# Kernel optimization log

Hardware: AMD Instinct MI355X
Metric: run time of the kernel (lower is better)

The kernel has to match this reference:

```python
import jax, jax.numpy as jnp
import numpy as np

EMBED_DIM = 4096
N_HEADS = 32
N_KV_HEADS = N_HEADS // 2
HEAD_DIM = EMBED_DIM // N_HEADS
MAX_SEQ_LEN = 4096


def setup_inputs() -> dict:
    key = jax.random.key(0)
    k1, k2, k3, k4, k5 = jax.random.split(key, 5)
    b, s = 1, 2048
    x = jax.random.normal(k1, (b, s, EMBED_DIM), dtype=jnp.float32)
    # rotary frequencies: theta=10000, angles[t, i] = t * 10000^{-2i/head_dim}
    inv_freq = 1.0 / (10000.0 ** (np.arange(0, HEAD_DIM, 2, dtype=np.float32) / HEAD_DIM))
    t = np.arange(MAX_SEQ_LEN, dtype=np.float32)
    ang = np.outer(t, inv_freq)  # [max_seq, head_dim/2]
    freqs_cis = jnp.asarray(np.stack([np.cos(ang), np.sin(ang)], axis=-1))  # [max_seq, hd/2, 2]
    scale = 0.02
    wq = jax.random.normal(k2, (EMBED_DIM, EMBED_DIM), dtype=jnp.float32) * scale
    wk = jax.random.normal(k3, (EMBED_DIM, N_KV_HEADS * HEAD_DIM), dtype=jnp.float32) * scale
    wv = jax.random.normal(k4, (EMBED_DIM, N_KV_HEADS * HEAD_DIM), dtype=jnp.float32) * scale
    wo = jax.random.normal(k5, (EMBED_DIM, EMBED_DIM), dtype=jnp.float32) * scale
    return {"x": x, "freqs_cis": freqs_cis, "wq": wq, "wk": wk, "wv": wv, "wo": wo, "start_pos": 0}


def _apply_rope(t, cos, sin):
    # t: [b, s, h, hd]; cos/sin: [1, s, 1, hd/2]
    tr = t.reshape(*t.shape[:-1], HEAD_DIM // 2, 2)
    t0, t1 = tr[..., 0], tr[..., 1]
    o0 = t0 * cos - t1 * sin
    o1 = t0 * sin + t1 * cos
    return jnp.stack([o0, o1], axis=-1).reshape(t.shape)


def reference(x, freqs_cis, wq, wk, wv, wo, start_pos):
    b, s, _ = x.shape
    q = (x @ wq).reshape(b, s, N_HEADS, HEAD_DIM)
    k = (x @ wk).reshape(b, s, N_KV_HEADS, HEAD_DIM)
    v = (x @ wv).reshape(b, s, N_KV_HEADS, HEAD_DIM)
    rep = N_HEADS // N_KV_HEADS
    k = jnp.repeat(k, rep, axis=2)  # GQA: expand KV heads (matches repeat_interleave)
    v = jnp.repeat(v, rep, axis=2)
    fc = freqs_cis[start_pos:start_pos + s]  # [s, hd/2, 2]
    cos = fc[None, :, None, :, 0]
    sin = fc[None, :, None, :, 1]
    q = _apply_rope(q, cos, sin)
    k = _apply_rope(k, cos, sin)
    # [b, h, s, hd]
    q = q.transpose(0, 2, 1, 3)
    k = k.transpose(0, 2, 1, 3)
    v = v.transpose(0, 2, 1, 3)
    scale = 1.0 / jnp.sqrt(jnp.float32(HEAD_DIM))
    scores = jnp.einsum("bhqd,bhkd->bhqk", q, k) * scale
    causal = jnp.tril(jnp.ones((s, s), dtype=bool))
    scores = jnp.where(causal[None, None], scores, jnp.finfo(scores.dtype).min)
    probs = jax.nn.softmax(scores, axis=-1)
    out = jnp.einsum("bhqk,bhkd->bhqd", probs, v)
    out = out.transpose(0, 2, 1, 3).reshape(b, s, EMBED_DIM)
    return out @ wo
```

## Files before the change

kernel.cpp:

```cpp
#include <hip/hip_runtime.h>
#include <stdint.h>

typedef unsigned short u16;
typedef __bf16 bf16x8 __attribute__((ext_vector_type(8)));
typedef float f32x4 __attribute__((ext_vector_type(4)));

#define SEQ   2048
#define EMBED 4096
#define KDIM  4096
#define NH    32
#define NKV   16
#define HD    128
#define KVW   2048

__device__ __forceinline__ float bf2f(u16 u) {
  union { uint32_t u; float f; } v; v.u = ((uint32_t)u) << 16; return v.f;
}
__device__ __forceinline__ u16 f2bf(float f) {
  union { float f; uint32_t u; } v; v.f = f;
  return (u16)((v.u + 0x7FFFu + ((v.u >> 16) & 1u)) >> 16);
}
__device__ __forceinline__ void g2l16(const u16* g, u16* l) {
  __builtin_amdgcn_global_load_lds(
      (const __attribute__((address_space(1))) uint32_t*)g,
      (__attribute__((address_space(3))) uint32_t*)l, 16, 0, 0);
}

__global__ __launch_bounds__(256) void convert_x(
    const float* __restrict__ X, u16* __restrict__ Xb, int nquad) {
  for (int i = blockIdx.x * 256 + threadIdx.x; i < nquad;
       i += gridDim.x * 256) {
    float4 v = *(const float4*)(X + (size_t)i * 4);
    ushort4 o;
    o.x = f2bf(v.x); o.y = f2bf(v.y); o.z = f2bf(v.z); o.w = f2bf(v.w);
    *(ushort4*)(Xb + (size_t)i * 4) = o;
  }
}

__global__ __launch_bounds__(256) void transpose_cvt(
    const float* __restrict__ W, u16* __restrict__ Wt, int K, int N) {
  __shared__ u16 tile[64][68];
  const int t = threadIdx.x;
  const int n0 = blockIdx.x * 64, k0 = blockIdx.y * 64;
#pragma unroll
  for (int i = 0; i < 4; i++) {
    int c = i * 256 + t;
    int r = c >> 4, cq = c & 15;
    float4 v = *(const float4*)(W + (size_t)(k0 + r) * N + n0 + cq * 4);
    tile[r][cq * 4 + 0] = f2bf(v.x); tile[r][cq * 4 + 1] = f2bf(v.y);
    tile[r][cq * 4 + 2] = f2bf(v.z); tile[r][cq * 4 + 3] = f2bf(v.w);
  }
  __syncthreads();
#pragma unroll
  for (int i = 0; i < 4; i++) {
    int c = i * 256 + t;
    int rn = c >> 4, cq = c & 15;
    ushort4 v;
    v.x = tile[cq * 4 + 0][rn];
    v.y = tile[cq * 4 + 1][rn];
    v.z = tile[cq * 4 + 2][rn];
    v.w = tile[cq * 4 + 3][rn];
    *(ushort4*)(Wt + (size_t)(n0 + rn) * K + k0 + cq * 4) = v;
  }
}

__global__ __launch_bounds__(512, 2) void gemm8_qkv(
    const u16* __restrict__ A,
    const u16* __restrict__ B0, const u16* __restrict__ B1,
    const u16* __restrict__ B2,
    u16* __restrict__ Qo, u16* __restrict__ Ko, u16* __restrict__ Vt) {
  __shared__ __align__(16) u16 As[2][256 * 64];
  __shared__ __align__(16) u16 Bs[2][256 * 64];
  const int t = threadIdx.x;
  const int lane = t & 63;
  const int w = t >> 6;
  const int wr = w >> 2;
  const int wc = w & 3;
  const int g = lane >> 4;
  const int l15 = lane & 15;

  const int bid = blockIdx.x;
  const int swz = (bid & 7) * 32 + (bid >> 3);
  const int mb = swz & 7;
  const int nb = swz >> 3;
  const int m0 = mb * 256;

  const u16* Bt; int nrow0;
  if (nb < 16)      { Bt = B0; nrow0 = nb * 256; }
  else if (nb < 24) { Bt = B1; nrow0 = (nb - 16) * 256; }
  else              { Bt = B2; nrow0 = (nb - 24) * 256; }

  auto stageA = [&](int buf, int kt, int h) {
#pragma unroll
    for (int i = 0; i < 2; i++) {
      int c = i * 512 + t;
      int row = c >> 3, sp = c & 7;
      int col = (sp ^ (row & 7)) << 3;
      g2l16(A + (size_t)(m0 + h * 128 + row) * KDIM + kt + col,
            &As[buf][h * 8192 + c * 8]);
    }
  };
  auto stageB = [&](int buf, int kt, int h) {
#pragma unroll
    for (int i = 0; i < 2; i++) {
      int c = i * 512 + t;
      int row = c >> 3, sp = c & 7;
      int col = (sp ^ (row & 7)) << 3;
      g2l16(Bt + (size_t)(nrow0 + h * 128 + row) * KDIM + kt + col,
            &Bs[buf][h * 8192 + c * 8]);
    }
  };

  f32x4 acc[8][4];
#pragma unroll
  for (int i = 0; i < 8; i++)
#pragma unroll
    for (int j = 0; j < 4; j++) acc[i][j] = (f32x4){0.f, 0.f, 0.f, 0.f};

  stageA(0, 0, 0); stageA(0, 0, 1);
  stageB(0, 0, 0); stageB(0, 0, 1);
  stageA(1, 64, 0); stageA(1, 64, 1);
  asm volatile("s_waitcnt vmcnt(4)" ::: "memory");
  __builtin_amdgcn_s_barrier();

  const int NT = KDIM / 64;
  for (int ti = 0; ti < NT; ++ti) {
    const int cur = ti & 1;
    const u16* Asc = As[cur];
    const u16* Bsc = Bs[cur];
    const int ktn  = (ti + 1) * 64;
    const int ktn2 = (ti + 2) * 64;
    bf16x8 a0[2][4], a1[2][4], b0[2][2], b1[2][2];

#pragma unroll
    for (int kk = 0; kk < 2; kk++)
#pragma unroll
      for (int mi = 0; mi < 4; mi++) {
        int r = wr * 128 + mi * 16 + l15;
        int slot = (kk * 4 + g) ^ (r & 7);
        a0[kk][mi] = *(const bf16x8*)(Asc + r * 64 + slot * 8);
      }
#pragma unroll
    for (int kk = 0; kk < 2; kk++)
#pragma unroll
      for (int ni = 0; ni < 2; ni++) {
        int r = wc * 64 + ni * 16 + l15;
        int slot = (kk * 4 + g) ^ (r & 7);
        b0[kk][ni] = *(const bf16x8*)(Bsc + r * 64 + slot * 8);
      }
    if (ti + 1 < NT) stageB(cur ^ 1, ktn, 0);
    __builtin_amdgcn_s_barrier();
    asm volatile("s_waitcnt lgkmcnt(0)" ::: "memory");
    __builtin_amdgcn_sched_barrier(0);
    __builtin_amdgcn_s_setprio(1);
#pragma unroll
    for (int mi = 0; mi < 4; mi++)
#pragma unroll
      for (int ni = 0; ni < 2; ni++)
#pragma unroll
        for (int kk = 0; kk < 2; kk++)
          acc[mi][ni] = __builtin_amdgcn_mfma_f32_16x16x32_bf16(
              a0[kk][mi], b0[kk][ni], acc[mi][ni], 0, 0, 0);
    __builtin_amdgcn_s_setprio(0);
    __builtin_amdgcn_s_barrier();

#pragma unroll
    for (int kk = 0; kk < 2; kk++)
#pragma unroll
      for (int ni = 0; ni < 2; ni++) {
        int r = wc * 64 + (ni + 2) * 16 + l15;
        int slot = (kk * 4 + g) ^ (r & 7);
        b1[kk][ni] = *(const bf16x8*)(Bsc + r * 64 + slot * 8);
      }
    if (ti + 1 < NT) stageB(cur ^ 1, ktn, 1);
    __builtin_amdgcn_s_barrier();
    asm volatile("s_waitcnt lgkmcnt(0)" ::: "memory");
    __builtin_amdgcn_sched_barrier(0);
    __builtin_amdgcn_s_setprio(1);
#pragma unroll
    for (int mi = 0; mi < 4; mi++)
#pragma unroll
      for (int ni = 0; ni < 2; ni++)
#pragma unroll
        for (int kk = 0; kk < 2; kk++)
          acc[mi][ni + 2] = __builtin_amdgcn_mfma_f32_16x16x32_bf16(
              a0[kk][mi], b1[kk][ni], acc[mi][ni + 2], 0, 0, 0);
    __builtin_amdgcn_s_setprio(0);
    __builtin_amdgcn_s_barrier();

#pragma unroll
    for (int kk = 0; kk < 2; kk++)
#pragma unroll
      for (int mi = 0; mi < 4; mi++) {
        int r = wr * 128 + 64 + mi * 16 + l15;
        int slot = (kk * 4 + g) ^ (r & 7);
        a1[kk][mi] = *(const bf16x8*)(Asc + r * 64 + slot * 8);
      }
    __builtin_amdgcn_s_barrier();
    asm volatile("s_waitcnt lgkmcnt(0)" ::: "memory");
    __builtin_amdgcn_sched_barrier(0);
    __builtin_amdgcn_s_setprio(1);
#pragma unroll
    for (int mi = 0; mi < 4; mi++)
#pragma unroll
      for (int ni = 0; ni < 2; ni++)
#pragma unroll
        for (int kk = 0; kk < 2; kk++)
          acc[mi + 4][ni + 2] = __builtin_amdgcn_mfma_f32_16x16x32_bf16(
              a1[kk][mi], b1[kk][ni], acc[mi + 4][ni + 2], 0, 0, 0);
    __builtin_amdgcn_s_setprio(0);
    __builtin_amdgcn_s_barrier();

    if (ti + 2 < NT) { stageA(cur, ktn2, 0); stageA(cur, ktn2, 1); }
    __builtin_amdgcn_s_barrier();
    __builtin_amdgcn_s_setprio(1);
#pragma unroll
    for (int mi = 0; mi < 4; mi++)
#pragma unroll
      for (int ni = 0; ni < 2; ni++)
#pragma unroll
        for (int kk = 0; kk < 2; kk++)
          acc[mi + 4][ni] = __builtin_amdgcn_mfma_f32_16x16x32_bf16(
              a1[kk][mi], b0[kk][ni], acc[mi + 4][ni], 0, 0, 0);
    __builtin_amdgcn_s_setprio(0);
    if (ti + 2 < NT)      asm volatile("s_waitcnt vmcnt(4)" ::: "memory");
    else if (ti + 1 < NT) asm volatile("s_waitcnt vmcnt(0)" ::: "memory");
    __builtin_amdgcn_s_barrier();
  }

#pragma unroll
  for (int mi = 0; mi < 8; mi++) {
#pragma unroll
    for (int ni = 0; ni < 4; ni++) {
      int rowg = m0 + wr * 128 + mi * 16 + g * 4;
      int ncol = nb * 256 + wc * 64 + ni * 16 + l15;
      if (nb < 16) {
#pragma unroll
        for (int r = 0; r < 4; r++)
          Qo[(size_t)(rowg + r) * EMBED + ncol] = f2bf(acc[mi][ni][r]);
      } else if (nb < 24) {
        int nc = ncol - 4096;
#pragma unroll
        for (int r = 0; r < 4; r++)
          Ko[(size_t)(rowg + r) * KVW + nc] = f2bf(acc[mi][ni][r]);
      } else {
        int nc = ncol - 6144;
        ushort4 v;
        v.x = f2bf(acc[mi][ni][0]); v.y = f2bf(acc[mi][ni][1]);
        v.z = f2bf(acc[mi][ni][2]); v.w = f2bf(acc[mi][ni][3]);
        *(ushort4*)(Vt + (size_t)nc * SEQ + rowg) = v;
      }
    }
  }
}

__global__ __launch_bounds__(256) void gemm_bt_f32(
    const u16* __restrict__ A, const u16* __restrict__ Bt,
    float* __restrict__ Cf) {
  __shared__ u16 As[128 * 64];
  __shared__ u16 Bs[128 * 64];
  const int t = threadIdx.x;
  const int lane = t & 63;
  const int w = t >> 6;
  const int wr = w >> 1, wc = w & 1;
  const int g = lane >> 4;
  const int l15 = lane & 15;

  const int flat = blockIdx.x + (int)gridDim.x * blockIdx.y;
  const int swz = (flat & 7) * 64 + (flat >> 3);
  const int m0 = (swz & 15) * 128;
  const int nb = swz >> 4;
  const int nrow0 = nb * 128;

  f32x4 acc[4][4];
#pragma unroll
  for (int i = 0; i < 4; i++)
#pragma unroll
    for (int j = 0; j < 4; j++) acc[i][j] = (f32x4){0.f, 0.f, 0.f, 0.f};

  for (int kt = 0; kt < KDIM; kt += 64) {
#pragma unroll
    for (int i = 0; i < 4; i++) {
      int c = i * 256 + t;
      int row = c >> 3, sp = c & 7;
      int col = ((sp ^ (row & 7)) << 3);
      g2l16(A  + (size_t)(m0 + row)    * KDIM + kt + col, As + c * 8);
      g2l16(Bt + (size_t)(nrow0 + row) * KDIM + kt + col, Bs + c * 8);
    }
    __syncthreads();
#pragma unroll
    for (int kk = 0; kk < 2; kk++) {
      bf16x8 af[4], bfr[4];
#pragma unroll
      for (int mi = 0; mi < 4; mi++) {
        int r = wr * 64 + mi * 16 + l15;
        int ps = (kk * 4 + g) ^ (r & 7);
        af[mi] = *(const bf16x8*)(As + r * 64 + ps * 8);
      }
#pragma unroll
      for (int ni = 0; ni < 4; ni++) {
        int r = wc * 64 + ni * 16 + l15;
        int ps = (kk * 4 + g) ^ (r & 7);
        bfr[ni] = *(const bf16x8*)(Bs + r * 64 + ps * 8);
      }
#pragma unroll
      for (int mi = 0; mi < 4; mi++)
#pragma unroll
        for (int ni = 0; ni < 4; ni++)
          acc[mi][ni] = __builtin_amdgcn_mfma_f32_16x16x32_bf16(
              af[mi], bfr[ni], acc[mi][ni], 0, 0, 0);
    }
    __syncthreads();
  }

#pragma unroll
  for (int mi = 0; mi < 4; mi++)
#pragma unroll
    for (int ni = 0; ni < 4; ni++) {
      int rowg = m0 + wr * 64 + mi * 16 + g * 4;
      int ncol = nb * 128 + wc * 64 + ni * 16 + l15;
#pragma unroll
      for (int r = 0; r < 4; r++)
        Cf[(size_t)(rowg + r) * 4096 + ncol] = acc[mi][ni][r];
    }
}

__global__ __launch_bounds__(256) void rope_kernel(
    u16* __restrict__ Q, u16* __restrict__ Kb,
    const float* __restrict__ freqs, const int* __restrict__ start_pos) {
  const int sp = start_pos[0];
  const float qscale = 0.08838834764831845f;
  const int total_q = SEQ * EMBED / 2;
  const int total_k = SEQ * KVW / 2;
  const int total = total_q + total_k;
  for (int idx = blockIdx.x * 256 + threadIdx.x; idx < total;
       idx += gridDim.x * 256) {
    u16* buf; int row, pi; bool isq = idx < total_q;
    if (isq) { row = idx >> 11; pi = idx & 2047; buf = Q + (size_t)row * EMBED; }
    else { int j = idx - total_q; row = j >> 10; pi = j & 1023; buf = Kb + (size_t)row * KVW; }
    int i = pi & 63;
    float2 cs = *(const float2*)(freqs + (size_t)(sp + row) * 128 + i * 2);
    float c = cs.x, s = cs.y;
    ushort2 tv = *(ushort2*)(buf + pi * 2);
    float t0 = bf2f(tv.x), t1 = bf2f(tv.y);
    float o0 = t0 * c - t1 * s;
    float o1 = t0 * s + t1 * c;
    if (isq) { o0 *= qscale; o1 *= qscale; }
    ushort2 o; o.x = f2bf(o0); o.y = f2bf(o1);
    *(ushort2*)(buf + pi * 2) = o;
  }
}

__global__ __launch_bounds__(256, 4) void attn_kernel(
    const u16* __restrict__ Q, const u16* __restrict__ Kb,
    const u16* __restrict__ Vt, u16* __restrict__ O) {
  __shared__ __align__(16) u16 KV[16384];
  __shared__ u16 Ps[4][16 * 72];

  const int t = threadIdx.x;
  const int lane = t & 63;
  const int w = t >> 6;
  const int g = lane >> 4;
  const int l15 = lane & 15;
  const int bid = blockIdx.x;
  const int qb = 31 - (bid >> 5);
  const int h = bid & 31;
  const int hk = h >> 1;

  auto stageK = [&](int kv) {
#pragma unroll
    for (int i = 0; i < 4; i++) {
      int c = i * 256 + t;
      int row = c >> 4, spp = c & 15;
      int col = ((spp ^ (row & 7)) << 3);
      g2l16(Kb + (size_t)(kv * 64 + row) * KVW + hk * HD + col, &KV[c * 8]);
    }
  };
  auto stageV = [&](int kv) {
#pragma unroll
    for (int i = 0; i < 4; i++) {
      int c = i * 256 + t;
      int row = c >> 3, spp = c & 7;
      int col = ((spp ^ (row & 7)) << 3);
      g2l16(Vt + (size_t)(hk * HD + row) * SEQ + kv * 64 + col,
            &KV[8192 + c * 8]);
    }
  };

#pragma unroll
  for (int i = 0; i < 4; i++) {
    int c = i * 256 + t;
    int row = c >> 4, spp = c & 15;
    int col = ((spp ^ (row & 7)) << 3);
    g2l16(Q + (size_t)(qb * 64 + row) * EMBED + h * HD + col, &KV[c * 8]);
  }
  asm volatile("s_waitcnt vmcnt(0)" ::: "memory");
  __builtin_amdgcn_s_barrier();

  bf16x8 qf[4];
  {
    int r = w * 16 + l15;
#pragma unroll
    for (int kk = 0; kk < 4; kk++) {
      int ps = (kk * 4 + g) ^ (r & 7);
      qf[kk] = *(const bf16x8*)(&KV[r * 128 + ps * 8]);
    }
  }
  asm volatile("s_waitcnt lgkmcnt(0)" ::: "memory");
  __builtin_amdgcn_s_barrier();

  f32x4 oacc[8];
#pragma unroll
  for (int i = 0; i < 8; i++) oacc[i] = (f32x4){0.f, 0.f, 0.f, 0.f};
  float mrow = -1e30f, lrow = 0.f;
  const int qg = qb * 64 + w * 16 + l15;

  for (int kv = 0; kv <= qb; kv++) {
    stageK(kv); stageV(kv);
    asm volatile("s_waitcnt vmcnt(0)" ::: "memory");
    __builtin_amdgcn_s_barrier();

    f32x4 sfragT[4];
    __builtin_amdgcn_s_setprio(1);
#pragma unroll
    for (int ni = 0; ni < 4; ni++) {
      f32x4 s = (f32x4){0.f, 0.f, 0.f, 0.f};
      int r = ni * 16 + l15;
#pragma unroll
      for (int kk = 0; kk < 4; kk++) {
        int ps = (kk * 4 + g) ^ (r & 7);
        bf16x8 a = *(const bf16x8*)(&KV[r * 128 + ps * 8]);
        s = __builtin_amdgcn_mfma_f32_16x16x32_bf16(a, qf[kk], s, 0, 0, 0);
      }
      sfragT[ni] = s;
    }
    __builtin_amdgcn_s_setprio(0);

    if (kv == qb) {
#pragma unroll
      for (int ni = 0; ni < 4; ni++) {
        int colg = kv * 64 + ni * 16 + g * 4;
#pragma unroll
        for (int r = 0; r < 4; r++)
          if (colg + r > qg) sfragT[ni][r] = -1e30f;
      }
    }

    float m16 = sfragT[0][0];
#pragma unroll
    for (int ni = 0; ni < 4; ni++)
#pragma unroll
      for (int r = 0; r < 4; r++) m16 = fmaxf(m16, sfragT[ni][r]);
    m16 = fmaxf(m16, __shfl_xor(m16, 16));
    m16 = fmaxf(m16, __shfl_xor(m16, 32));
    float mnew = fmaxf(mrow, m16);
    float sc = __expf(mrow - mnew);
    mrow = mnew;

    float rsum = 0.f;
#pragma unroll
    for (int ni = 0; ni < 4; ni++) {
#pragma unroll
      for (int r = 0; r < 4; r++) {
        float p = __expf(sfragT[ni][r] - mrow);
        rsum += p;
        Ps[w][l15 * 72 + ni * 16 + g * 4 + r] = f2bf(p);
      }
    }
    rsum += __shfl_xor(rsum, 16);
    rsum += __shfl_xor(rsum, 32);
    lrow = lrow * sc + rsum;

    float scr[4];
#pragma unroll
    for (int r = 0; r < 4; r++) scr[r] = __shfl(sc, g * 4 + r, 64);
#pragma unroll
    for (int nf = 0; nf < 8; nf++)
#pragma unroll
      for (int r = 0; r < 4; r++) oacc[nf][r] *= scr[r];

    asm volatile("s_waitcnt lgkmcnt(0)" ::: "memory");

    bf16x8 pa[2];
#pragma unroll
    for (int kk = 0; kk < 2; kk++)
      pa[kk] = *(const bf16x8*)(&Ps[w][l15 * 72 + kk * 32 + g * 8]);
    __builtin_amdgcn_s_setprio(1);
#pragma unroll
    for (int nf = 0; nf < 8; nf++) {
      int r = nf * 16 + l15;
#pragma unroll
      for (int kk = 0; kk < 2; kk++) {
        int ps = (kk * 4 + g) ^ (r & 7);
        bf16x8 b = *(const bf16x8*)(&KV[8192 + r * 64 + ps * 8]);
        oacc[nf] = __builtin_amdgcn_mfma_f32_16x16x32_bf16(pa[kk], b, oacc[nf], 0, 0, 0);
      }
    }
    __builtin_amdgcn_s_setprio(0);
    __builtin_amdgcn_s_barrier();
  }

  float lr[4];
#pragma unroll
  for (int r = 0; r < 4; r++) lr[r] = __shfl(lrow, g * 4 + r, 64);
#pragma unroll
  for (int nf = 0; nf < 8; nf++) {
#pragma unroll
    for (int r = 0; r < 4; r++) {
      int rowg = qb * 64 + w * 16 + g * 4 + r;
      float v = oacc[nf][r] / lr[r];
      O[(size_t)rowg * EMBED + h * HD + nf * 16 + l15] = f2bf(v);
    }
  }
}

extern "C" void kernel_launch(void* const* d_in, const int* in_sizes, int n_in,
                              void* d_out, int out_size, void* d_ws, size_t ws_size,
                              hipStream_t stream) {
  const float* x  = (const float*)d_in[0];
  const float* fc = (const float*)d_in[1];
  const float* wq = (const float*)d_in[2];
  const float* wk = (const float*)d_in[3];
  const float* wv = (const float*)d_in[4];
  const float* wo = (const float*)d_in[5];
  const int* sp = (const int*)d_in[6];

  char* ws = (char*)d_ws;
  u16* wqT = (u16*)(ws);
  u16* wkT = (u16*)(ws + 33554432ull);
  u16* wvT = (u16*)(ws + 50331648ull);
  u16* woT = (u16*)(ws + 67108864ull);
  u16* xb  = (u16*)(ws + 100663296ull);
  u16* Qb  = (u16*)(ws + 117440512ull);
  u16* Kb  = (u16*)(ws + 134217728ull);
  u16* Vt  = (u16*)(ws + 142606336ull);
  u16* Ob  = (u16*)(ws + 150994944ull);

  convert_x<<<dim3(2048), 256, 0, stream>>>(x, xb, SEQ * EMBED / 4);
  transpose_cvt<<<dim3(64, 64), 256, 0, stream>>>(wq, wqT, 4096, 4096);
  transpose_cvt<<<dim3(32, 64), 256, 0, stream>>>(wk, wkT, 4096, 2048);
  transpose_cvt<<<dim3(32, 64), 256, 0, stream>>>(wv, wvT, 4096, 2048);
  transpose_cvt<<<dim3(64, 64), 256, 0, stream>>>(wo, woT, 4096, 4096);

  gemm8_qkv<<<dim3(256), 512, 0, stream>>>(xb, wqT, wkT, wvT, Qb, Kb, Vt);
  rope_kernel<<<dim3(2048), 256, 0, stream>>>(Qb, Kb, fc, sp);
  attn_kernel<<<dim3(1024), 256, 0, stream>>>(Qb, Kb, Vt, Ob);
  gemm_bt_f32<<<dim3(16, 32), 256, 0, stream>>>(Ob, woT, (float*)d_out);
}
```

Baseline: 361.4 us.

## Deepen QKV GEMM prefetch and replace output GEMM with pipelined 8-wave kernel

The QKV GEMM now prefetches both A and B tiles two iterations ahead, reorders its MFMA quadrants, and relaxes its vmcnt wait to match, so global loads overlap more compute. The output projection GEMM is rewritten from a single-buffered 4-wave 128x128 kernel with __syncthreads into an 8-wave 128x256 double-buffered kernel using direct-to-LDS loads, split MFMA phases and setprio. This aims to hide memory latency and cut barrier stalls in the projection GEMMs, at the cost of more LDS per block and fewer blocks.

```diff
diff --git a/kernel.cpp b/kernel.cpp
--- a/kernel.cpp
+++ b/kernel.cpp
@@ -120,7 +120,8 @@
   stageA(0, 0, 0); stageA(0, 0, 1);
   stageB(0, 0, 0); stageB(0, 0, 1);
   stageA(1, 64, 0); stageA(1, 64, 1);
-  asm volatile("s_waitcnt vmcnt(4)" ::: "memory");
+  stageB(1, 64, 0); stageB(1, 64, 1);
+  asm volatile("s_waitcnt vmcnt(8)" ::: "memory");
   __builtin_amdgcn_s_barrier();
 
   const int NT = KDIM / 64;
@@ -128,7 +129,6 @@
     const int cur = ti & 1;
     const u16* Asc = As[cur];
     const u16* Bsc = Bs[cur];
-    const int ktn  = (ti + 1) * 64;
     const int ktn2 = (ti + 2) * 64;
     bf16x8 a0[2][4], a1[2][4], b0[2][2], b1[2][2];
 
@@ -148,7 +148,6 @@
         int slot = (kk * 4 + g) ^ (r & 7);
         b0[kk][ni] = *(const bf16x8*)(Bsc + r * 64 + slot * 8);
       }
-    if (ti + 1 < NT) stageB(cur ^ 1, ktn, 0);
     __builtin_amdgcn_s_barrier();
     asm volatile("s_waitcnt lgkmcnt(0)" ::: "memory");
     __builtin_amdgcn_sched_barrier(0);
@@ -161,6 +160,29 @@
         for (int kk = 0; kk < 2; kk++)
           acc[mi][ni] = __builtin_amdgcn_mfma_f32_16x16x32_bf16(
               a0[kk][mi], b0[kk][ni], acc[mi][ni], 0, 0, 0);
+    __builtin_amdgcn_s_setprio(0);
+    __builtin_amdgcn_s_barrier();
+
+#pragma unroll
+    for (int kk = 0; kk < 2; kk++)
+#pragma unroll
+      for (int mi = 0; mi < 4; mi++) {
+        int r = wr * 128 + 64 + mi * 16 + l15;
+        int slot = (kk * 4 + g) ^ (r & 7);
+        a1[kk][mi] = *(const bf16x8*)(Asc + r * 64 + slot * 8);
+      }
+    __builtin_amdgcn_s_barrier();
+    asm volatile("s_waitcnt lgkmcnt(0)" ::: "memory");
+    __builtin_amdgcn_sched_barrier(0);
+    __builtin_amdgcn_s_setprio(1);
+#pragma unroll
+    for (int mi = 0; mi < 4; mi++)
+#pragma unroll
+      for (int ni = 0; ni < 2; ni++)
+#pragma unroll
+        for (int kk = 0; kk < 2; kk++)
+          acc[mi + 4][ni] = __builtin_amdgcn_mfma_f32_16x16x32_bf16(
+              a1[kk][mi], b0[kk][ni], acc[mi + 4][ni], 0, 0, 0);
     __builtin_amdgcn_s_setprio(0);
     __builtin_amdgcn_s_barrier();
 
@@ -172,10 +194,24 @@
         int slot = (kk * 4 + g) ^ (r & 7);
         b1[kk][ni] = *(const bf16x8*)(Bsc + r * 64 + slot * 8);
       }
-    if (ti + 1 < NT) stageB(cur ^ 1, ktn, 1);
+    if (ti + 2 < NT) { stageA(cur, ktn2, 0); stageA(cur, ktn2, 1); }
     __builtin_amdgcn_s_barrier();
     asm volatile("s_waitcnt lgkmcnt(0)" ::: "memory");
     __builtin_amdgcn_sched_barrier(0);
+    __builtin_amdgcn_s_setprio(1);
+#pragma unroll
+    for (int mi = 0; mi < 4; mi++)
+#pragma unroll
+      for (int ni = 0; ni < 2; ni++)
+#pragma unroll
+        for (int kk = 0; kk < 2; kk++)
+          acc[mi + 4][ni + 2] = __builtin_amdgcn_mfma_f32_16x16x32_bf16(
+              a1[kk][mi], b1[kk][ni], acc[mi + 4][ni + 2], 0, 0, 0);
+    __builtin_amdgcn_s_setprio(0);
+    __builtin_amdgcn_s_barrier();
+
+    if (ti + 2 < NT) { stageB(cur, ktn2, 0); stageB(cur, ktn2, 1); }
+    __builtin_amdgcn_s_barrier();
     __builtin_amdgcn_s_setprio(1);
 #pragma unroll
     for (int mi = 0; mi < 4; mi++)
@@ -186,44 +222,7 @@
           acc[mi][ni + 2] = __builtin_amdgcn_mfma_f32_16x16x32_bf16(
               a0[kk][mi], b1[kk][ni], acc[mi][ni + 2], 0, 0, 0);
     __builtin_amdgcn_s_setprio(0);
-    __builtin_amdgcn_s_barrier();
-
-#pragma unroll
-    for (int kk = 0; kk < 2; kk++)
-#pragma unroll
-      for (int mi = 0; mi < 4; mi++) {
-        int r = wr * 128 + 64 + mi * 16 + l15;
-        int slot = (kk * 4 + g) ^ (r & 7);
-        a1[kk][mi] = *(const bf16x8*)(Asc + r * 64 + slot * 8);
-      }
-    __builtin_amdgcn_s_barrier();
-    asm volatile("s_waitcnt lgkmcnt(0)" ::: "memory");
-    __builtin_amdgcn_sched_barrier(0);
-    __builtin_amdgcn_s_setprio(1);
-#pragma unroll
-    for (int mi = 0; mi < 4; mi++)
-#pragma unroll
-      for (int ni = 0; ni < 2; ni++)
-#pragma unroll
-        for (int kk = 0; kk < 2; kk++)
-          acc[mi + 4][ni + 2] = __builtin_amdgcn_mfma_f32_16x16x32_bf16(
-              a1[kk][mi], b1[kk][ni], acc[mi + 4][ni + 2], 0, 0, 0);
-    __builtin_amdgcn_s_setprio(0);
-    __builtin_amdgcn_s_barrier();
-
-    if (ti + 2 < NT) { stageA(cur, ktn2, 0); stageA(cur, ktn2, 1); }
-    __builtin_amdgcn_s_barrier();
-    __builtin_amdgcn_s_setprio(1);
-#pragma unroll
-    for (int mi = 0; mi < 4; mi++)
-#pragma unroll
-      for (int ni = 0; ni < 2; ni++)
-#pragma unroll
-        for (int kk = 0; kk < 2; kk++)
-          acc[mi + 4][ni] = __builtin_amdgcn_mfma_f32_16x16x32_bf16(
-              a1[kk][mi], b0[kk][ni], acc[mi + 4][ni], 0, 0, 0);
-    __builtin_amdgcn_s_setprio(0);
-    if (ti + 2 < NT)      asm volatile("s_waitcnt vmcnt(4)" ::: "memory");
+    if (ti + 2 < NT)      asm volatile("s_waitcnt vmcnt(8)" ::: "memory");
     else if (ti + 1 < NT) asm volatile("s_waitcnt vmcnt(0)" ::: "memory");
     __builtin_amdgcn_s_barrier();
   }
@@ -254,23 +253,44 @@
   }
 }
 
-__global__ __launch_bounds__(256) void gemm_bt_f32(
+__global__ __launch_bounds__(512, 2) void gemm8_op(
     const u16* __restrict__ A, const u16* __restrict__ Bt,
     float* __restrict__ Cf) {
-  __shared__ u16 As[128 * 64];
-  __shared__ u16 Bs[128 * 64];
+  __shared__ __align__(16) u16 As[2][128 * 64];
+  __shared__ __align__(16) u16 Bs[2][256 * 64];
   const int t = threadIdx.x;
   const int lane = t & 63;
   const int w = t >> 6;
-  const int wr = w >> 1, wc = w & 1;
+  const int wr = w >> 2;
+  const int wc = w & 3;
   const int g = lane >> 4;
   const int l15 = lane & 15;
 
-  const int flat = blockIdx.x + (int)gridDim.x * blockIdx.y;
-  const int swz = (flat & 7) * 64 + (flat >> 3);
-  const int m0 = (swz & 15) * 128;
+  const int bid = blockIdx.x;
+  const int swz = (bid & 7) * 32 + (bid >> 3);
+  const int mb = swz & 15;
   const int nb = swz >> 4;
-  const int nrow0 = nb * 128;
+  const int m0 = mb * 128;
+  const int nrow0 = nb * 256;
+
+  auto stageA = [&](int buf, int kt) {
+#pragma unroll
+    for (int i = 0; i < 2; i++) {
+      int c = i * 512 + t;
+      int row = c >> 3, sp = c & 7;
+      int col = (sp ^ (row & 7)) << 3;
+      g2l16(A + (size_t)(m0 + row) * KDIM + kt + col, &As[buf][c * 8]);
+    }
+  };
+  auto stageB = [&](int buf, int kt) {
+#pragma unroll
+    for (int i = 0; i < 4; i++) {
+      int c = i * 512 + t;
+      int row = c >> 3, sp = c & 7;
+      int col = (sp ^ (row & 7)) << 3;
+      g2l16(Bt + (size_t)(nrow0 + row) * KDIM + kt + col, &Bs[buf][c * 8]);
+    }
+  };
 
   f32x4 acc[4][4];
 #pragma unroll
@@ -278,39 +298,73 @@
 #pragma unroll
     for (int j = 0; j < 4; j++) acc[i][j] = (f32x4){0.f, 0.f, 0.f, 0.f};
 
-  for (int kt = 0; kt < KDIM; kt += 64) {
-#pragma unroll
-    for (int i = 0; i < 4; i++) {
-      int c = i * 256 + t;
-      int row = c >> 3, sp = c & 7;
-      int col = ((sp ^ (row & 7)) << 3);
-      g2l16(A  + (size_t)(m0 + row)    * KDIM + kt + col, As + c * 8);
-      g2l16(Bt + (size_t)(nrow0 + row) * KDIM + kt + col, Bs + c * 8);
-    }
-    __syncthreads();
-#pragma unroll
-    for (int kk = 0; kk < 2; kk++) {
-      bf16x8 af[4], bfr[4];
+  stageA(0, 0); stageB(0, 0);
+  stageA(1, 64); stageB(1, 64);
+  asm volatile("s_waitcnt vmcnt(6)" ::: "memory");
+  __builtin_amdgcn_s_barrier();
+
+  const int NT = KDIM / 64;
+  for (int ti = 0; ti < NT; ++ti) {
+    const int cur = ti & 1;
+    const u16* Asc = As[cur];
+    const u16* Bsc = Bs[cur];
+    const int ktn2 = (ti + 2) * 64;
+    bf16x8 a[2][4], b0[2][2], b1[2][2];
+
+#pragma unroll
+    for (int kk = 0; kk < 2; kk++)
 #pragma unroll
       for (int mi = 0; mi < 4; mi++) {
         int r = wr * 64 + mi * 16 + l15;
-        int ps = (kk * 4 + g) ^ (r & 7);
-        af[mi] = *(const bf16x8*)(As + r * 64 + ps * 8);
-      }
-#pragma unroll
-      for (int ni = 0; ni < 4; ni++) {
+        int slot = (kk * 4 + g) ^ (r & 7);
+        a[kk][mi] = *(const bf16x8*)(Asc + r * 64 + slot * 8);
+      }
+#pragma unroll
+    for (int kk = 0; kk < 2; kk++)
+#pragma unroll
+      for (int ni = 0; ni < 2; ni++) {
         int r = wc * 64 + ni * 16 + l15;
-        int ps = (kk * 4 + g) ^ (r & 7);
-        bfr[ni] = *(const bf16x8*)(Bs + r * 64 + ps * 8);
-      }
-#pragma unroll
-      for (int mi = 0; mi < 4; mi++)
-#pragma unroll
-        for (int ni = 0; ni < 4; ni++)
+        int slot = (kk * 4 + g) ^ (r & 7);
+        b0[kk][ni] = *(const bf16x8*)(Bsc + r * 64 + slot * 8);
+      }
+#pragma unroll
+    for (int kk = 0; kk < 2; kk++)
+#pragma unroll
+      for (int ni = 0; ni < 2; ni++) {
+        int r = wc * 64 + (ni + 2) * 16 + l15;
+        int slot = (kk * 4 + g) ^ (r & 7);
+        b1[kk][ni] = *(const bf16x8*)(Bsc + r * 64 + slot * 8);
+      }
+    __builtin_amdgcn_s_barrier();
+    asm volatile("s_waitcnt lgkmcnt(0)" ::: "memory");
+    __builtin_amdgcn_sched_barrier(0);
+    __builtin_amdgcn_s_setprio(1);
+#pragma unroll
+    for (int mi = 0; mi < 4; mi++)
+#pragma unroll
+      for (int ni = 0; ni < 2; ni++)
+#pragma unroll
+        for (int kk = 0; kk < 2; kk++)
           acc[mi][ni] = __builtin_amdgcn_mfma_f32_16x16x32_bf16(
-              af[mi], bfr[ni], acc[mi][ni], 0, 0, 0);
-    }
-    __syncthreads();
+              a[kk][mi], b0[kk][ni], acc[mi][ni], 0, 0, 0);
+    __builtin_amdgcn_s_setprio(0);
+    __builtin_amdgcn_s_barrier();
+
+    if (ti + 2 < NT) { stageA(cur, ktn2); stageB(cur, ktn2); }
+    __builtin_amdgcn_s_barrier();
+    __builtin_amdgcn_s_setprio(1);
+#pragma unroll
+    for (int mi = 0; mi < 4; mi++)
+#pragma unroll
+      for (int ni = 0; ni < 2; ni++)
+#pragma unroll
+        for (int kk = 0; kk < 2; kk++)
+          acc[mi][ni + 2] = __builtin_amdgcn_mfma_f32_16x16x32_bf16(
+              a[kk][mi], b1[kk][ni], acc[mi][ni + 2], 0, 0, 0);
+    __builtin_amdgcn_s_setprio(0);
+    if (ti + 2 < NT)      asm volatile("s_waitcnt vmcnt(6)" ::: "memory");
+    else if (ti + 1 < NT) asm volatile("s_waitcnt vmcnt(0)" ::: "memory");
+    __builtin_amdgcn_s_barrier();
   }
 
 #pragma unroll
@@ -318,7 +372,7 @@
 #pragma unroll
     for (int ni = 0; ni < 4; ni++) {
       int rowg = m0 + wr * 64 + mi * 16 + g * 4;
-      int ncol = nb * 128 + wc * 64 + ni * 16 + l15;
+      int ncol = nb * 256 + wc * 64 + ni * 16 + l15;
 #pragma unroll
       for (int r = 0; r < 4; r++)
         Cf[(size_t)(rowg + r) * 4096 + ncol] = acc[mi][ni][r];
@@ -545,5 +599,5 @@
   gemm8_qkv<<<dim3(256), 512, 0, stream>>>(xb, wqT, wkT, wvT, Qb, Kb, Vt);
   rope_kernel<<<dim3(2048), 256, 0, stream>>>(Qb, Kb, fc, sp);
   attn_kernel<<<dim3(1024), 256, 0, stream>>>(Qb, Kb, Vt, Ob);
-  gemm_bt_f32<<<dim3(16, 32), 256, 0, stream>>>(Ob, woT, (float*)d_out);
-}
+  gemm8_op<<<dim3(256), 512, 0, stream>>>(Ob, woT, (float*)d_out);
+}
```

Result: no change. 360.5 us (-0.3%).
